# Performance work log

Measured on AMD Instinct MI355X. Metric: run time of the kernel, lower is better.

Reference implementation:

```python
import jax, jax.numpy as jnp
import numpy as np

B, T, C, H = 4, 2048, 1024, 16
D = C // H

def setup_inputs() -> dict:
    key = jax.random.key(0)
    ks = jax.random.split(key, 9)
    s = 0.02
    return {
        'x':  jax.random.normal(ks[0], (B, T, C), jnp.float32),
        'Wq': jax.random.normal(ks[1], (C, C), jnp.float32) * s,
        'bq': jnp.zeros((C,), jnp.float32),
        'Wk': jax.random.normal(ks[2], (C, C), jnp.float32) * s,
        'bk': jnp.zeros((C,), jnp.float32),
        'Wv': jax.random.normal(ks[3], (C, C), jnp.float32) * s,
        'bv': jnp.zeros((C,), jnp.float32),
        'Wp': jax.random.normal(ks[4], (C, C), jnp.float32) * s,
        'bp': jnp.zeros((C,), jnp.float32),
    }

def reference(x, Wq, bq, Wk, bk, Wv, bv, Wp, bp):
    # linear projections: torch Linear stores weight [out,in]; here W is [in,out]
    q = (x @ Wq + bq).reshape(B, T, H, D).transpose(0, 2, 1, 3)  # [B,H,T,D]
    k = (x @ Wk + bk).reshape(B, T, H, D).transpose(0, 2, 1, 3)
    v = (x @ Wv + bv).reshape(B, T, H, D).transpose(0, 2, 1, 3)
    att = jnp.einsum('bhqd,bhkd->bhqk', q, k) * (1.0 / jnp.sqrt(jnp.float32(D)))
    causal = jnp.tril(jnp.ones((T, T), bool))  # mask[:T,:T]
    att = jnp.where(causal[None, None], att, -jnp.inf)
    att = jax.nn.softmax(att, axis=-1)
    attn_save = att  # dropout p=0 (eval) => identity
    y = jnp.einsum('bhqk,bhkd->bhqd', att, v)
    y = y.transpose(0, 2, 1, 3).reshape(B, T, C)
    y = y @ Wp + bp  # resid dropout p=0 => identity
    return (y, attn_save)
```

## Files before the change

kernel.cpp:

```cpp
#include <hip/hip_runtime.h>


using bf16x8 = __attribute__((ext_vector_type(8))) short;
using f32x4  = __attribute__((ext_vector_type(4))) float;

__device__ __forceinline__ unsigned short f2bf(float f) {
    union { float f; unsigned u; } v; v.f = f;
    unsigned u = v.u;
    return (unsigned short)((u + 0x7fffu + ((u >> 16) & 1u)) >> 16);
}

__global__ __launch_bounds__(256) void convert_x(const float* __restrict__ x,
                                                 short* __restrict__ xb, int n4) {
    int i = blockIdx.x * 256 + threadIdx.x;
    if (i < n4) {
        float4 v = ((const float4*)x)[i];
        ushort4 o;
        o.x = f2bf(v.x); o.y = f2bf(v.y); o.z = f2bf(v.z); o.w = f2bf(v.w);
        ((ushort4*)xb)[i] = o;
    }
}

__global__ __launch_bounds__(256) void transpose_w(const float* __restrict__ Wq,
                                                   const float* __restrict__ Wk,
                                                   const float* __restrict__ Wv,
                                                   const float* __restrict__ Wp,
                                                   short* __restrict__ Wt) {
    __shared__ float tile[32][33];
    int z = blockIdx.z;
    const float* src = (z == 0) ? Wq : (z == 1) ? Wk : (z == 2) ? Wv : Wp;
    short* dst = Wt + (size_t)z * 1024 * 1024;
    int n0 = blockIdx.x * 32, k0 = blockIdx.y * 32;
    int tx = threadIdx.x, ty = threadIdx.y;
#pragma unroll
    for (int r = 0; r < 32; r += 8)
        tile[ty + r][tx] = src[(size_t)(k0 + ty + r) * 1024 + n0 + tx];
    __syncthreads();
#pragma unroll
    for (int r = 0; r < 32; r += 8)
        dst[(size_t)(n0 + ty + r) * 1024 + k0 + tx] = (short)f2bf(tile[tx][ty + r]);
}

template <int MODE>
__global__ __launch_bounds__(256) void gemm_bt(
    const short* __restrict__ A, const short* __restrict__ Bt,
    const float* __restrict__ bias0, const float* __restrict__ bias1,
    const float* __restrict__ bias2,
    short* __restrict__ Qh, short* __restrict__ Kh, short* __restrict__ Vth,
    float* __restrict__ Yout) {
    constexpr int K = 1024;
    __shared__ short As[128 * 40];
    __shared__ short Bs[128 * 40];
    int tid = threadIdx.x;
    int m0 = blockIdx.y * 128;
    int n0 = blockIdx.x * 128;
    int srow = tid >> 2;
    int scol = (tid & 3) << 3;
    int lane = tid & 63;
    int wave = tid >> 6;
    int wm = (wave >> 1) << 6;
    int wn = (wave & 1) << 6;
    int lr = lane & 15;
    int lq = lane >> 4;
    f32x4 acc[4][4];
#pragma unroll
    for (int i = 0; i < 4; i++)
#pragma unroll
        for (int j = 0; j < 4; j++) acc[i][j] = (f32x4){0.f, 0.f, 0.f, 0.f};

    for (int k0 = 0; k0 < K; k0 += 32) {
        __syncthreads();
#pragma unroll
        for (int p = 0; p < 2; ++p) {
            int row = p * 64 + srow;
            *(uint4*)&As[row * 40 + scol] =
                *(const uint4*)&A[(size_t)(m0 + row) * K + k0 + scol];
            *(uint4*)&Bs[row * 40 + scol] =
                *(const uint4*)&Bt[(size_t)(n0 + row) * K + k0 + scol];
        }
        __syncthreads();
        bf16x8 af[4], bfr[4];
#pragma unroll
        for (int i = 0; i < 4; i++)
            af[i] = *(const bf16x8*)&As[(wm + i * 16 + lr) * 40 + lq * 8];
#pragma unroll
        for (int j = 0; j < 4; j++)
            bfr[j] = *(const bf16x8*)&Bs[(wn + j * 16 + lr) * 40 + lq * 8];
#pragma unroll
        for (int i = 0; i < 4; i++)
#pragma unroll
            for (int j = 0; j < 4; j++)
                acc[i][j] = __builtin_amdgcn_mfma_f32_16x16x32_bf16(af[i], bfr[j],
                                                                    acc[i][j], 0, 0, 0);
    }

#pragma unroll
    for (int i = 0; i < 4; i++) {
        int m_base = m0 + wm + i * 16 + lq * 4;
#pragma unroll
        for (int j = 0; j < 4; j++) {
            int n_g = n0 + wn + j * 16 + lr;
            if (MODE == 0) {
                int which = n_g >> 10;
                int nn = n_g & 1023;
                int h = nn >> 6, d = nn & 63;
                const float* bs = (which == 0) ? bias0 : (which == 1) ? bias1 : bias2;
                float bv_ = bs[nn];
#pragma unroll
                for (int r = 0; r < 4; r++) {
                    int m_g = m_base + r;
                    int b = m_g >> 11, t = m_g & 2047;
                    float v = acc[i][j][r] + bv_;
                    size_t head = (size_t)(b * 16 + h);
                    if (which == 0)
                        Qh[(head * 2048 + t) * 64 + d] = (short)f2bf(v * 0.125f);
                    else if (which == 1)
                        Kh[(head * 2048 + t) * 64 + d] = (short)f2bf(v);
                    else
                        Vth[(head * 64 + d) * 2048 + t] = (short)f2bf(v);
                }
            } else {
                float bv_ = bias0[n_g];
#pragma unroll
                for (int r = 0; r < 4; r++) {
                    int m_g = m_base + r;
                    Yout[(size_t)m_g * 1024 + n_g] = acc[i][j][r] + bv_;
                }
            }
        }
    }
}

__global__ __launch_bounds__(256) void attn_kernel(
    const short* __restrict__ Qh, const short* __restrict__ Kh,
    const short* __restrict__ Vt, float* __restrict__ att, short* __restrict__ Yb) {
    __shared__ short Pl[4][16 * 40];
    int tid = threadIdx.x;
    int lane = tid & 63;
    int wave = tid >> 6;
    int qt = blockIdx.x * 4 + wave;
    int bh = blockIdx.y;
    int b = bh >> 4, h = bh & 15;
    int q0 = qt << 4;
    const short* Qp = Qh + (size_t)bh * (2048 * 64);
    const short* Kp = Kh + (size_t)bh * (2048 * 64);
    const short* Vp = Vt + (size_t)bh * (2048 * 64);
    float* attp = att + (size_t)bh * 2048 * 2048;
    int lr = lane & 15, lq = lane >> 4;

    bf16x8 qa0 = *(const bf16x8*)&Qp[(q0 + lr) * 64 + lq * 8];
    bf16x8 qa1 = *(const bf16x8*)&Qp[(q0 + lr) * 64 + 32 + lq * 8];

    f32x4 lsum = {0.f, 0.f, 0.f, 0.f};
    for (int kt = 0; kt <= qt; ++kt) {
        const short* kr = &Kp[(kt * 16 + lr) * 64 + lq * 8];
        bf16x8 kb0 = *(const bf16x8*)kr;
        bf16x8 kb1 = *(const bf16x8*)(kr + 32);
        f32x4 s = __builtin_amdgcn_mfma_f32_16x16x32_bf16(
            qa0, kb0, (f32x4){0.f, 0.f, 0.f, 0.f}, 0, 0, 0);
        s = __builtin_amdgcn_mfma_f32_16x16x32_bf16(qa1, kb1, s, 0, 0, 0);
        int colg = kt * 16 + lr;
#pragma unroll
        for (int r = 0; r < 4; r++) {
            int rowg = q0 + lq * 4 + r;
            lsum[r] += (colg <= rowg) ? __expf(s[r]) : 0.0f;
        }
    }
#pragma unroll
    for (int m = 1; m < 16; m <<= 1) {
#pragma unroll
        for (int r = 0; r < 4; r++) lsum[r] += __shfl_xor(lsum[r], m, 64);
    }
    float rl[4];
#pragma unroll
    for (int r = 0; r < 4; r++) rl[r] = 1.0f / lsum[r];

    f32x4 o[4];
#pragma unroll
    for (int j = 0; j < 4; j++) o[j] = (f32x4){0.f, 0.f, 0.f, 0.f};
    short* Pw = Pl[wave];
    int nchunk = (qt >> 1) + 1;
    for (int c = 0; c < nchunk; ++c) {
#pragma unroll
        for (int half = 0; half < 2; ++half) {
            int kt = c * 2 + half;
            if (kt <= qt) {
                const short* kr = &Kp[(kt * 16 + lr) * 64 + lq * 8];
                bf16x8 kb0 = *(const bf16x8*)kr;
                bf16x8 kb1 = *(const bf16x8*)(kr + 32);
                f32x4 s = __builtin_amdgcn_mfma_f32_16x16x32_bf16(
                    qa0, kb0, (f32x4){0.f, 0.f, 0.f, 0.f}, 0, 0, 0);
                s = __builtin_amdgcn_mfma_f32_16x16x32_bf16(qa1, kb1, s, 0, 0, 0);
                int colg = kt * 16 + lr;
#pragma unroll
                for (int r = 0; r < 4; r++) {
                    int rowg = q0 + lq * 4 + r;
                    float p = (colg <= rowg) ? __expf(s[r]) * rl[r] : 0.0f;
                    attp[(size_t)rowg * 2048 + colg] = p;
                    Pw[(lq * 4 + r) * 40 + half * 16 + lr] = (short)f2bf(p);
                }
            } else {
#pragma unroll
                for (int r = 0; r < 4; r++)
                    Pw[(lq * 4 + r) * 40 + half * 16 + lr] = 0;
            }
        }
        __threadfence_block();
        bf16x8 pf = *(const bf16x8*)&Pw[lr * 40 + lq * 8];
#pragma unroll
        for (int j = 0; j < 4; j++) {
            bf16x8 vf = *(const bf16x8*)&Vp[(j * 16 + lr) * 2048 + c * 32 + lq * 8];
            o[j] = __builtin_amdgcn_mfma_f32_16x16x32_bf16(pf, vf, o[j], 0, 0, 0);
        }
        __threadfence_block();
    }

    int zc0 = (qt + 1) * 16;
    for (int r = 0; r < 16; ++r) {
        float* rowp = attp + (size_t)(q0 + r) * 2048;
        for (int c = zc0 + lane * 4; c < 2048; c += 256)
            *(float4*)(rowp + c) = (float4){0.f, 0.f, 0.f, 0.f};
    }

#pragma unroll
    for (int j = 0; j < 4; j++)
#pragma unroll
        for (int r = 0; r < 4; r++)
            Yb[(size_t)(b * 2048 + q0 + lq * 4 + r) * 1024 + h * 64 + j * 16 + lr] =
                (short)f2bf(o[j][r]);
}

extern "C" void kernel_launch(void* const* d_in, const int* in_sizes, int n_in,
                              void* d_out, int out_size, void* d_ws, size_t ws_size,
                              hipStream_t stream) {
    const float* x  = (const float*)d_in[0];
    const float* Wq = (const float*)d_in[1];
    const float* bq = (const float*)d_in[2];
    const float* Wk = (const float*)d_in[3];
    const float* bk = (const float*)d_in[4];
    const float* Wv = (const float*)d_in[5];
    const float* bv = (const float*)d_in[6];
    const float* Wp = (const float*)d_in[7];
    const float* bp = (const float*)d_in[8];

    float* y = (float*)d_out;
    float* att = y + (size_t)4 * 2048 * 1024;

    char* ws = (char*)d_ws;
    short* xb = (short*)(ws);
    short* Wt = (short*)(ws + 16777216);
    short* Qh = (short*)(ws + 25165824);
    short* Kh = (short*)(ws + 41943040);
    short* Vt = (short*)(ws + 58720256);
    short* Yb = (short*)(ws + 75497472);

    convert_x<<<8192, 256, 0, stream>>>(x, xb, 2097152);
    transpose_w<<<dim3(32, 32, 4), dim3(32, 8), 0, stream>>>(Wq, Wk, Wv, Wp, Wt);
    gemm_bt<0><<<dim3(24, 64), 256, 0, stream>>>(xb, Wt, bq, bk, bv, Qh, Kh, Vt,
                                                 (float*)nullptr);
    attn_kernel<<<dim3(32, 64), 256, 0, stream>>>(Qh, Kh, Vt, att, Yb);
    gemm_bt<1><<<dim3(8, 64), 256, 0, stream>>>(Yb, Wt + (size_t)3072 * 1024, bp,
                                                (const float*)nullptr,
                                                (const float*)nullptr,
                                                (short*)nullptr, (short*)nullptr,
                                                (short*)nullptr, y);
}
```

Baseline: 1.834 ms.

## Balance causal attention work and coalesce attention-matrix stores via LDS staging

```diff
diff --git a/kernel.cpp b/kernel.cpp
--- a/kernel.cpp
+++ b/kernel.cpp
@@ -134,100 +134,124 @@
 __global__ __launch_bounds__(256) void attn_kernel(
     const short* __restrict__ Qh, const short* __restrict__ Kh,
     const short* __restrict__ Vt, float* __restrict__ att, short* __restrict__ Yb) {
-    __shared__ short Pl[4][16 * 40];
+    __shared__ __attribute__((aligned(16))) short Pl[2][4][16 * 40];
+    __shared__ __attribute__((aligned(16))) float Pf[2][4][16 * 36];
     int tid = threadIdx.x;
     int lane = tid & 63;
     int wave = tid >> 6;
-    int qt = blockIdx.x * 4 + wave;
+    int wv = blockIdx.x * 4 + wave;
     int bh = blockIdx.y;
     int b = bh >> 4, h = bh & 15;
-    int q0 = qt << 4;
     const short* Qp = Qh + (size_t)bh * (2048 * 64);
     const short* Kp = Kh + (size_t)bh * (2048 * 64);
     const short* Vp = Vt + (size_t)bh * (2048 * 64);
     float* attp = att + (size_t)bh * 2048 * 2048;
     int lr = lane & 15, lq = lane >> 4;
 
-    bf16x8 qa0 = *(const bf16x8*)&Qp[(q0 + lr) * 64 + lq * 8];
-    bf16x8 qa1 = *(const bf16x8*)&Qp[(q0 + lr) * 64 + 32 + lq * 8];
-
-    f32x4 lsum = {0.f, 0.f, 0.f, 0.f};
-    for (int kt = 0; kt <= qt; ++kt) {
-        const short* kr = &Kp[(kt * 16 + lr) * 64 + lq * 8];
-        bf16x8 kb0 = *(const bf16x8*)kr;
-        bf16x8 kb1 = *(const bf16x8*)(kr + 32);
-        f32x4 s = __builtin_amdgcn_mfma_f32_16x16x32_bf16(
-            qa0, kb0, (f32x4){0.f, 0.f, 0.f, 0.f}, 0, 0, 0);
-        s = __builtin_amdgcn_mfma_f32_16x16x32_bf16(qa1, kb1, s, 0, 0, 0);
-        int colg = kt * 16 + lr;
-#pragma unroll
-        for (int r = 0; r < 4; r++) {
-            int rowg = q0 + lq * 4 + r;
-            lsum[r] += (colg <= rowg) ? __expf(s[r]) : 0.0f;
-        }
-    }
-#pragma unroll
-    for (int m = 1; m < 16; m <<= 1) {
-#pragma unroll
-        for (int r = 0; r < 4; r++) lsum[r] += __shfl_xor(lsum[r], m, 64);
-    }
-    float rl[4];
-#pragma unroll
-    for (int r = 0; r < 4; r++) rl[r] = 1.0f / lsum[r];
-
-    f32x4 o[4];
-#pragma unroll
-    for (int j = 0; j < 4; j++) o[j] = (f32x4){0.f, 0.f, 0.f, 0.f};
-    short* Pw = Pl[wave];
-    int nchunk = (qt >> 1) + 1;
-    for (int c = 0; c < nchunk; ++c) {
-#pragma unroll
-        for (int half = 0; half < 2; ++half) {
-            int kt = c * 2 + half;
-            if (kt <= qt) {
-                const short* kr = &Kp[(kt * 16 + lr) * 64 + lq * 8];
-                bf16x8 kb0 = *(const bf16x8*)kr;
-                bf16x8 kb1 = *(const bf16x8*)(kr + 32);
-                f32x4 s = __builtin_amdgcn_mfma_f32_16x16x32_bf16(
-                    qa0, kb0, (f32x4){0.f, 0.f, 0.f, 0.f}, 0, 0, 0);
-                s = __builtin_amdgcn_mfma_f32_16x16x32_bf16(qa1, kb1, s, 0, 0, 0);
-                int colg = kt * 16 + lr;
-#pragma unroll
-                for (int r = 0; r < 4; r++) {
-                    int rowg = q0 + lq * 4 + r;
-                    float p = (colg <= rowg) ? __expf(s[r]) * rl[r] : 0.0f;
-                    attp[(size_t)rowg * 2048 + colg] = p;
-                    Pw[(lq * 4 + r) * 40 + half * 16 + lr] = (short)f2bf(p);
+#pragma unroll 1
+    for (int pass = 0; pass < 2; ++pass) {
+        int qt = pass ? (127 - wv) : wv;
+        int q0 = qt << 4;
+
+        bf16x8 qa0 = *(const bf16x8*)&Qp[(q0 + lr) * 64 + lq * 8];
+        bf16x8 qa1 = *(const bf16x8*)&Qp[(q0 + lr) * 64 + 32 + lq * 8];
+
+        f32x4 lsum = {0.f, 0.f, 0.f, 0.f};
+        for (int kt = 0; kt < qt; ++kt) {
+            const short* kr = &Kp[(kt * 16 + lr) * 64 + lq * 8];
+            bf16x8 kb0 = *(const bf16x8*)kr;
+            bf16x8 kb1 = *(const bf16x8*)(kr + 32);
+            f32x4 s = __builtin_amdgcn_mfma_f32_16x16x32_bf16(
+                qa0, kb0, (f32x4){0.f, 0.f, 0.f, 0.f}, 0, 0, 0);
+            s = __builtin_amdgcn_mfma_f32_16x16x32_bf16(qa1, kb1, s, 0, 0, 0);
+#pragma unroll
+            for (int r = 0; r < 4; r++) lsum[r] += __expf(s[r]);
+        }
+        {
+            const short* kr = &Kp[(qt * 16 + lr) * 64 + lq * 8];
+            bf16x8 kb0 = *(const bf16x8*)kr;
+            bf16x8 kb1 = *(const bf16x8*)(kr + 32);
+            f32x4 s = __builtin_amdgcn_mfma_f32_16x16x32_bf16(
+                qa0, kb0, (f32x4){0.f, 0.f, 0.f, 0.f}, 0, 0, 0);
+            s = __builtin_amdgcn_mfma_f32_16x16x32_bf16(qa1, kb1, s, 0, 0, 0);
+#pragma unroll
+            for (int r = 0; r < 4; r++)
+                lsum[r] += (lr <= lq * 4 + r) ? __expf(s[r]) : 0.0f;
+        }
+#pragma unroll
+        for (int m = 1; m < 16; m <<= 1) {
+#pragma unroll
+            for (int r = 0; r < 4; r++) lsum[r] += __shfl_xor(lsum[r], m, 64);
+        }
+        float rl[4];
+#pragma unroll
+        for (int r = 0; r < 4; r++) rl[r] = 1.0f / lsum[r];
+
+        f32x4 o[4];
+#pragma unroll
+        for (int j = 0; j < 4; j++) o[j] = (f32x4){0.f, 0.f, 0.f, 0.f};
+        int nchunk = (qt >> 1) + 1;
+        for (int c = 0; c < nchunk; ++c) {
+            short* Pw = Pl[c & 1][wave];
+            float* Pfw = Pf[c & 1][wave];
+#pragma unroll
+            for (int half = 0; half < 2; ++half) {
+                int kt = c * 2 + half;
+                if (kt <= qt) {
+                    const short* kr = &Kp[(kt * 16 + lr) * 64 + lq * 8];
+                    bf16x8 kb0 = *(const bf16x8*)kr;
+                    bf16x8 kb1 = *(const bf16x8*)(kr + 32);
+                    f32x4 s = __builtin_amdgcn_mfma_f32_16x16x32_bf16(
+                        qa0, kb0, (f32x4){0.f, 0.f, 0.f, 0.f}, 0, 0, 0);
+                    s = __builtin_amdgcn_mfma_f32_16x16x32_bf16(qa1, kb1, s, 0, 0, 0);
+                    int colg = kt * 16 + lr;
+#pragma unroll
+                    for (int r = 0; r < 4; r++) {
+                        int rowg = q0 + lq * 4 + r;
+                        float p = (colg <= rowg) ? __expf(s[r]) * rl[r] : 0.0f;
+                        Pw[(lq * 4 + r) * 40 + half * 16 + lr] = (short)f2bf(p);
+                        Pfw[(lq * 4 + r) * 36 + half * 16 + lr] = p;
+                    }
+                } else {
+#pragma unroll
+                    for (int r = 0; r < 4; r++) {
+                        Pw[(lq * 4 + r) * 40 + half * 16 + lr] = 0;
+                        Pfw[(lq * 4 + r) * 36 + half * 16 + lr] = 0.0f;
+                    }
                 }
-            } else {
-#pragma unroll
-                for (int r = 0; r < 4; r++)
-                    Pw[(lq * 4 + r) * 40 + half * 16 + lr] = 0;
-            }
-        }
-        __threadfence_block();
-        bf16x8 pf = *(const bf16x8*)&Pw[lr * 40 + lq * 8];
-#pragma unroll
-        for (int j = 0; j < 4; j++) {
-            bf16x8 vf = *(const bf16x8*)&Vp[(j * 16 + lr) * 2048 + c * 32 + lq * 8];
-            o[j] = __builtin_amdgcn_mfma_f32_16x16x32_bf16(pf, vf, o[j], 0, 0, 0);
-        }
-        __threadfence_block();
-    }
-
-    int zc0 = (qt + 1) * 16;
-    for (int r = 0; r < 16; ++r) {
-        float* rowp = attp + (size_t)(q0 + r) * 2048;
-        for (int c = zc0 + lane * 4; c < 2048; c += 256)
-            *(float4*)(rowp + c) = (float4){0.f, 0.f, 0.f, 0.f};
-    }
-
-#pragma unroll
-    for (int j = 0; j < 4; j++)
-#pragma unroll
-        for (int r = 0; r < 4; r++)
-            Yb[(size_t)(b * 2048 + q0 + lq * 4 + r) * 1024 + h * 64 + j * 16 + lr] =
-                (short)f2bf(o[j][r]);
+            }
+            asm volatile("s_waitcnt lgkmcnt(0)" ::: "memory");
+
+#pragma unroll
+            for (int it = 0; it < 2; ++it) {
+                int row = (it * 64 + lane) >> 3;
+                int c4 = (lane & 7) << 2;
+                float4 pv = *(const float4*)&Pfw[row * 36 + c4];
+                *(float4*)&attp[(size_t)(q0 + row) * 2048 + c * 32 + c4] = pv;
+            }
+
+            bf16x8 pfr = *(const bf16x8*)&Pw[lr * 40 + lq * 8];
+#pragma unroll
+            for (int j = 0; j < 4; j++) {
+                bf16x8 vf = *(const bf16x8*)&Vp[(j * 16 + lr) * 2048 + c * 32 + lq * 8];
+                o[j] = __builtin_amdgcn_mfma_f32_16x16x32_bf16(pfr, vf, o[j], 0, 0, 0);
+            }
+        }
+
+        int zc0 = nchunk * 32;
+        for (int r = 0; r < 16; ++r) {
+            float* rowp = attp + (size_t)(q0 + r) * 2048;
+            for (int c = zc0 + lane * 4; c < 2048; c += 256)
+                *(float4*)(rowp + c) = (float4){0.f, 0.f, 0.f, 0.f};
+        }
+
+#pragma unroll
+        for (int j = 0; j < 4; j++)
+#pragma unroll
+            for (int r = 0; r < 4; r++)
+                Yb[(size_t)(b * 2048 + q0 + lq * 4 + r) * 1024 + h * 64 + j * 16 + lr] =
+                    (short)f2bf(o[j][r]);
+    }
 }
 
 extern "C" void kernel_launch(void* const* d_in, const int* in_sizes, int n_in,
@@ -258,7 +282,7 @@
     transpose_w<<<dim3(32, 32, 4), dim3(32, 8), 0, stream>>>(Wq, Wk, Wv, Wp, Wt);
     gemm_bt<0><<<dim3(24, 64), 256, 0, stream>>>(xb, Wt, bq, bk, bv, Qh, Kh, Vt,
                                                  (float*)nullptr);
-    attn_kernel<<<dim3(32, 64), 256, 0, stream>>>(Qh, Kh, Vt, att, Yb);
+    attn_kernel<<<dim3(16, 64), 256, 0, stream>>>(Qh, Kh, Vt, att, Yb);
     gemm_bt<1><<<dim3(8, 64), 256, 0, stream>>>(Yb, Wt + (size_t)3072 * 1024, bp,
                                                 (const float*)nullptr,
                                                 (const float*)nullptr,
```

Result: faster. 1.634 ms (-10.9%).
